# Performance work log

Measured on AMD Instinct MI355X. Metric: run time of the kernel, lower is better.

Reference implementation:

```python
import jax, jax.numpy as jnp
import numpy as np

S, B, I, H = 512, 128, 256, 512  # seq_len, batch, input_size, hidden_size


def setup_inputs() -> dict:
    key = jax.random.key(0)
    ks = jax.random.split(key, 5)
    # Gates stacked in order (f, i, o, c), each Linear init'd like nn.Linear
    lim_w = 1.0 / np.sqrt(I)
    lim_u = 1.0 / np.sqrt(H)
    x = jax.random.normal(ks[0], (S, B, I), dtype=jnp.float32)
    W = jax.random.uniform(ks[1], (4 * H, I), minval=-lim_w, maxval=lim_w, dtype=jnp.float32)
    bW = jax.random.uniform(ks[2], (4 * H,), minval=-lim_w, maxval=lim_w, dtype=jnp.float32)
    U = jax.random.uniform(ks[3], (4 * H, H), minval=-lim_u, maxval=lim_u, dtype=jnp.float32)
    bU = jax.random.uniform(ks[4], (4 * H,), minval=-lim_u, maxval=lim_u, dtype=jnp.float32)
    return {"x": x, "W": W, "bW": bW, "U": U, "bU": bU}


def reference(x, W, bW, U, bU):
    """LSTM over time-major x. Gates stacked (f, i, o, c) along dim 0 of W/U.
    Returns (h_seq [S,B,H], h_final [B,H], c_final [B,H]).
    The original's bf/bi/bo/bc buffers are zeros and thus omitted."""
    Hh = U.shape[1]
    # Input projection for all timesteps + both Linear biases, done once.
    xg = jnp.einsum('sbi,gi->sbg', x, W) + bW + bU  # [S, B, 4H]

    def step(carry, xg_t):
        h, c = carry
        g = xg_t + h @ U.T  # [B, 4H]
        f = jax.nn.sigmoid(g[:, 0 * Hh:1 * Hh])
        i = jax.nn.sigmoid(g[:, 1 * Hh:2 * Hh])
        o = jax.nn.sigmoid(g[:, 2 * Hh:3 * Hh])
        cand = jnp.tanh(g[:, 3 * Hh:4 * Hh])
        c_new = f * c + i * cand
        h_new = o * jnp.tanh(c_new)
        return (h_new, c_new), h_new

    b = x.shape[1]
    init = (jnp.zeros((b, Hh), x.dtype), jnp.zeros((b, Hh), x.dtype))
    (h_fin, c_fin), h_seq = jax.lax.scan(step, init, xg)
    return h_seq, h_fin, c_fin
```

## Files before the change

### kernel.cpp

```cpp
#include <hip/hip_runtime.h>
#include <hip/hip_bf16.h>


#define S_LEN 512
#define BATCH 128
#define ISZ   256
#define HSZ   512

typedef __attribute__((ext_vector_type(8))) short  s16x8;
typedef __attribute__((ext_vector_type(4))) float  f32x4;

#define FLAG_BYTES 4096
#define HOFF   4096
#define HBYTES ((size_t)2 * BATCH * HSZ * 2)
#define XOFF   (HOFF + HBYTES)
#define XBYTES ((size_t)S_LEN * BATCH * ISZ * 2)
#define WS_NEED (XOFF + XBYTES)

__device__ __forceinline__ unsigned short f2bf(float f) {
    unsigned u = __float_as_uint(f);
    u += 0x7fffu + ((u >> 16) & 1u);
    return (unsigned short)(u >> 16);
}

__device__ __forceinline__ s16x8 ld8f_bf(const float* p) {
    f32x4 a = *(const f32x4*)p;
    f32x4 b = *(const f32x4*)(p + 4);
    s16x8 r;
    r[0] = (short)f2bf(a[0]); r[1] = (short)f2bf(a[1]);
    r[2] = (short)f2bf(a[2]); r[3] = (short)f2bf(a[3]);
    r[4] = (short)f2bf(b[0]); r[5] = (short)f2bf(b[1]);
    r[6] = (short)f2bf(b[2]); r[7] = (short)f2bf(b[3]);
    return r;
}

__global__ void __launch_bounds__(256, 1)
cvt_x_kernel(const float* __restrict__ x, unsigned short* __restrict__ xbf, int n8) {
    int i = blockIdx.x * blockDim.x + threadIdx.x;
    const int stride = gridDim.x * blockDim.x;
    for (; i < n8; i += stride)
        *(s16x8*)(xbf + (size_t)i * 8) = ld8f_bf(x + (size_t)i * 8);
}

#define MFMA_BF16 __builtin_amdgcn_mfma_f32_16x16x32_bf16

template <bool BIGWS>
__global__ void __launch_bounds__(256, 1)
lstm_kq(const float* __restrict__ x,
        const float* __restrict__ W,
        const float* __restrict__ bW,
        const float* __restrict__ U,
        const float* __restrict__ bU,
        float* __restrict__ out,
        unsigned char* __restrict__ ws)
{
    __shared__ float g_lds[2][4][16][68];

    const int tid  = threadIdx.x;
    const int bid  = blockIdx.x;
    const int grp  = bid & 7;
    const int wg   = bid >> 3;
    const int jBase = wg * 16;
    const int rBase = grp * 16;

    unsigned* flags = (unsigned*)ws;
    unsigned short* h0 = (unsigned short*)(ws + HOFF);
    unsigned short* h1 = h0 + BATCH * HSZ;
    const unsigned short* xbf = (const unsigned short*)(ws + XOFF);

    const int kq   = tid >> 6;
    const int lane = tid & 63;
    const int l15  = lane & 15;
    const int lq   = lane >> 4;
    const int arow = rBase + l15;

    s16x8 ub[4][4], wb[4][2];
    float bias[4];
    #pragma unroll
    for (int n = 0; n < 4; ++n) {
        const int gRow = n * HSZ + jBase + l15;
        bias[n] = (kq == 0) ? (bW[gRow] + bU[gRow]) : 0.f;
        #pragma unroll
        for (int ki = 0; ki < 4; ++ki)
            ub[n][ki] = ld8f_bf(U + (size_t)gRow * HSZ + kq * 128 + ki * 32 + lq * 8);
        #pragma unroll
        for (int ki = 0; ki < 2; ++ki)
            wb[n][ki] = ld8f_bf(W + (size_t)gRow * ISZ + kq * 64 + ki * 32 + lq * 8);
    }

    const int er = tid >> 4, ej = tid & 15;
    const int orow = rBase + er, ocol = jBase + ej;
    float cst = 0.f;

    for (int t = 0; t < S_LEN; ++t) {
        const int par = t & 1;
        f32x4 acc[4] = { { bias[0], bias[0], bias[0], bias[0] },
                         { bias[1], bias[1], bias[1], bias[1] },
                         { bias[2], bias[2], bias[2], bias[2] },
                         { bias[3], bias[3], bias[3], bias[3] } };

        #pragma unroll
        for (int ki = 0; ki < 2; ++ki) {
            s16x8 a;
            if constexpr (BIGWS)
                a = *(const s16x8*)(xbf + ((size_t)t * BATCH + arow) * ISZ
                                    + kq * 64 + ki * 32 + lq * 8);
            else
                a = ld8f_bf(x + ((size_t)t * BATCH + arow) * ISZ
                            + kq * 64 + ki * 32 + lq * 8);
            #pragma unroll
            for (int n = 0; n < 4; ++n)
                acc[n] = MFMA_BF16(a, wb[n][ki], acc[n], 0, 0, 0);
        }

        if (t > 0) {
            const unsigned* fp = flags + grp * 128 + kq * 32 + (lane & 31);
            const unsigned tgt = (unsigned)t;
            for (;;) {
                unsigned v;
                asm volatile("global_load_dword %0, %1, off sc0 sc1\n\t"
                             "s_waitcnt vmcnt(0)" : "=v"(v) : "v"(fp) : "memory");
                if (__all(v >= tgt)) break;
            }
            __builtin_amdgcn_sched_barrier(0);

            const unsigned short* hp = (par ? h0 : h1)
                                       + (size_t)arow * HSZ + kq * 128 + lq * 8;
            s16x8 f0, f1, f2, f3;
#define LDH(d, o) asm volatile("global_load_dwordx4 %0, %1, off offset:" o " sc0 sc1" \
                               : "=v"(d) : "v"(hp) : "memory")
            LDH(f0, "0"); LDH(f1, "64"); LDH(f2, "128"); LDH(f3, "192");
#undef LDH
            asm volatile("s_waitcnt vmcnt(2)" ::: "memory");
            __builtin_amdgcn_sched_barrier(0);
            #pragma unroll
            for (int n = 0; n < 4; ++n)
                acc[n] = MFMA_BF16(f0, ub[n][0], acc[n], 0, 0, 0);
            #pragma unroll
            for (int n = 0; n < 4; ++n)
                acc[n] = MFMA_BF16(f1, ub[n][1], acc[n], 0, 0, 0);
            asm volatile("s_waitcnt vmcnt(0)" ::: "memory");
            __builtin_amdgcn_sched_barrier(0);
            #pragma unroll
            for (int n = 0; n < 4; ++n)
                acc[n] = MFMA_BF16(f2, ub[n][2], acc[n], 0, 0, 0);
            #pragma unroll
            for (int n = 0; n < 4; ++n)
                acc[n] = MFMA_BF16(f3, ub[n][3], acc[n], 0, 0, 0);
        }

        #pragma unroll
        for (int n = 0; n < 4; ++n)
            #pragma unroll
            for (int r = 0; r < 4; ++r)
                g_lds[par][kq][lq * 4 + r][n * 16 + l15] = acc[n][r];
        __syncthreads();

        const float gf = g_lds[par][0][er][ej]      + g_lds[par][1][er][ej]
                       + g_lds[par][2][er][ej]      + g_lds[par][3][er][ej];
        const float gi = g_lds[par][0][er][16 + ej] + g_lds[par][1][er][16 + ej]
                       + g_lds[par][2][er][16 + ej] + g_lds[par][3][er][16 + ej];
        const float go = g_lds[par][0][er][32 + ej] + g_lds[par][1][er][32 + ej]
                       + g_lds[par][2][er][32 + ej] + g_lds[par][3][er][32 + ej];
        const float gc = g_lds[par][0][er][48 + ej] + g_lds[par][1][er][48 + ej]
                       + g_lds[par][2][er][48 + ej] + g_lds[par][3][er][48 + ej];

        const float fg = 1.f / (1.f + __expf(-gf));
        const float ig = 1.f / (1.f + __expf(-gi));
        const float og = 1.f / (1.f + __expf(-go));
        const float ec = __expf(-2.f * fabsf(gc));
        const float cd = copysignf((1.f - ec) / (1.f + ec), gc);
        cst = fg * cst + ig * cd;
        const float eh = __expf(-2.f * fabsf(cst));
        const float hn = og * copysignf((1.f - eh) / (1.f + eh), cst);

        if (t < S_LEN - 1) {
            unsigned hv = (unsigned)f2bf(hn);
            unsigned short* hd = (par ? h1 : h0) + (size_t)orow * HSZ + ocol;
            asm volatile("global_store_short %0, %1, off sc0 sc1"
                         :: "v"(hd), "v"(hv) : "memory");
            asm volatile("s_waitcnt vmcnt(0)" ::: "memory");
            if (lane == 0) {
                unsigned* fl = flags + grp * 128 + wg * 4 + kq;
                unsigned ep = (unsigned)(t + 1);
                asm volatile("global_store_dword %0, %1, off sc0 sc1"
                             :: "v"(fl), "v"(ep) : "memory");
            }
            out[((size_t)t * BATCH + orow) * HSZ + ocol] = hn;
        } else {
            out[((size_t)t * BATCH + orow) * HSZ + ocol] = hn;
            const size_t HSEQ = (size_t)S_LEN * BATCH * HSZ;
            out[HSEQ + (size_t)orow * HSZ + ocol] = hn;
            out[HSEQ + (size_t)BATCH * HSZ + (size_t)orow * HSZ + ocol] = cst;
        }
    }
}

extern "C" void kernel_launch(void* const* d_in, const int* in_sizes, int n_in,
                              void* d_out, int out_size, void* d_ws, size_t ws_size,
                              hipStream_t stream) {
    const float* x  = (const float*)d_in[0];
    const float* W  = (const float*)d_in[1];
    const float* bW = (const float*)d_in[2];
    const float* U  = (const float*)d_in[3];
    const float* bU = (const float*)d_in[4];
    float* out = (float*)d_out;
    unsigned char* ws = (unsigned char*)d_ws;

    hipMemsetAsync(ws, 0, FLAG_BYTES, stream);

    void* args[] = { (void*)&x, (void*)&W, (void*)&bW, (void*)&U, (void*)&bU,
                     (void*)&out, (void*)&ws };

    if (ws_size >= WS_NEED) {
        const int n8 = S_LEN * BATCH * ISZ / 8;
        cvt_x_kernel<<<2048, 256, 0, stream>>>(x, (unsigned short*)(ws + XOFF), n8);
        hipError_t e = hipLaunchCooperativeKernel((void*)lstm_kq<true>, dim3(256),
                                                  dim3(256), args, 0, stream);
        if (e != hipSuccess)
            lstm_kq<true><<<dim3(256), dim3(256), 0, stream>>>(x, W, bW, U, bU, out, ws);
    } else {
        hipError_t e = hipLaunchCooperativeKernel((void*)lstm_kq<false>, dim3(256),
                                                  dim3(256), args, 0, stream);
        if (e != hipSuccess)
            lstm_kq<false><<<dim3(256), dim3(256), 0, stream>>>(x, W, bW, U, bU, out, ws);
    }
}
```

Baseline: 1.323 ms.

## Tag hidden-state words with timestep to validate data without store fences

Each hidden-state value is now stored as a 32-bit word: the bf16 value in the low half and the producing timestep in the high half. Consumers spin-load their h slice and check every tag against the expected step, then repack the low halves into bf16 MFMA operands. This removes the store wait that used to sit between the h store and the flag store. The cost is twice the h bytes on every step, an extra validation and repack pass, and clearing the larger workspace at launch. The old flag polling loop still runs before the tag check.

```diff
diff --git a/kernel.cpp b/kernel.cpp
--- a/kernel.cpp
+++ b/kernel.cpp
@@ -7,20 +7,32 @@
 #define ISZ   256
 #define HSZ   512
 
-typedef __attribute__((ext_vector_type(8))) short  s16x8;
-typedef __attribute__((ext_vector_type(4))) float  f32x4;
+typedef __attribute__((ext_vector_type(8))) short    s16x8;
+typedef __attribute__((ext_vector_type(4))) float    f32x4;
+typedef __attribute__((ext_vector_type(4))) unsigned u32x4;
+typedef __attribute__((ext_vector_type(4))) int      i32x4;
 
 #define FLAG_BYTES 4096
-#define HOFF   4096
-#define HBYTES ((size_t)2 * BATCH * HSZ * 2)
-#define XOFF   (HOFF + HBYTES)
-#define XBYTES ((size_t)S_LEN * BATCH * ISZ * 2)
+#define HOFF    4096
+#define HXWORDS ((size_t)BATCH * HSZ)
+#define HXBYTES ((size_t)2 * BATCH * HSZ * 4)
+#define XOFF    (HOFF + HXBYTES)
+#define XBYTES  ((size_t)S_LEN * BATCH * ISZ * 2)
 #define WS_NEED (XOFF + XBYTES)
 
 __device__ __forceinline__ unsigned short f2bf(float f) {
     unsigned u = __float_as_uint(f);
     u += 0x7fffu + ((u >> 16) & 1u);
     return (unsigned short)(u >> 16);
+}
+
+__device__ __forceinline__ unsigned permb(unsigned a, unsigned b, unsigned sel) {
+#if __has_builtin(__builtin_amdgcn_perm)
+    return __builtin_amdgcn_perm(a, b, sel);
+#else
+    if (sel == 0x01000504u) return (a & 0xFFFFu) | (b << 16);
+    else                    return (a >> 16) | (b & 0xFFFF0000u);
+#endif
 }
 
 __device__ __forceinline__ s16x8 ld8f_bf(const float* p) {
@@ -46,13 +58,13 @@
 
 template <bool BIGWS>
 __global__ void __launch_bounds__(256, 1)
-lstm_kq(const float* __restrict__ x,
-        const float* __restrict__ W,
-        const float* __restrict__ bW,
-        const float* __restrict__ U,
-        const float* __restrict__ bU,
-        float* __restrict__ out,
-        unsigned char* __restrict__ ws)
+lstm_tagflag(const float* __restrict__ x,
+             const float* __restrict__ W,
+             const float* __restrict__ bW,
+             const float* __restrict__ U,
+             const float* __restrict__ bU,
+             float* __restrict__ out,
+             unsigned char* __restrict__ ws)
 {
     __shared__ float g_lds[2][4][16][68];
 
@@ -64,8 +76,7 @@
     const int rBase = grp * 16;
 
     unsigned* flags = (unsigned*)ws;
-    unsigned short* h0 = (unsigned short*)(ws + HOFF);
-    unsigned short* h1 = h0 + BATCH * HSZ;
+    unsigned* hx    = (unsigned*)(ws + HOFF);
     const unsigned short* xbf = (const unsigned short*)(ws + XOFF);
 
     const int kq   = tid >> 6;
@@ -124,23 +135,42 @@
             }
             __builtin_amdgcn_sched_barrier(0);
 
-            const unsigned short* hp = (par ? h0 : h1)
-                                       + (size_t)arow * HSZ + kq * 128 + lq * 8;
-            s16x8 f0, f1, f2, f3;
-#define LDH(d, o) asm volatile("global_load_dwordx4 %0, %1, off offset:" o " sc0 sc1" \
+            const unsigned* hp = hx + (size_t)((t - 1) & 1) * HXWORDS
+                                 + (size_t)arow * HSZ + kq * 128 + lq * 8;
+            const unsigned tt = ((unsigned)t << 16) | (unsigned)t;
+            u32x4 L0, L1, L2, L3, L4, L5, L6, L7;
+            for (;;) {
+#define LDT(d, o) asm volatile("global_load_dwordx4 %0, %1, off offset:" o " sc0 sc1" \
                                : "=v"(d) : "v"(hp) : "memory")
-            LDH(f0, "0"); LDH(f1, "64"); LDH(f2, "128"); LDH(f3, "192");
-#undef LDH
-            asm volatile("s_waitcnt vmcnt(2)" ::: "memory");
-            __builtin_amdgcn_sched_barrier(0);
+                LDT(L0, "0");   LDT(L1, "16");
+                LDT(L2, "128"); LDT(L3, "144");
+                LDT(L4, "256"); LDT(L5, "272");
+                LDT(L6, "384"); LDT(L7, "400");
+#undef LDT
+                asm volatile("s_waitcnt vmcnt(0)" ::: "memory");
+                __builtin_amdgcn_sched_barrier(0);
+                unsigned bad = 0;
+#define TCHK(A) { bad |= permb(A[0], A[1], 0x03020706u) ^ tt; \
+                  bad |= permb(A[2], A[3], 0x03020706u) ^ tt; }
+                TCHK(L0) TCHK(L1) TCHK(L2) TCHK(L3)
+                TCHK(L4) TCHK(L5) TCHK(L6) TCHK(L7)
+#undef TCHK
+                if (__all(bad == 0)) break;
+                __builtin_amdgcn_s_sleep(1);
+            }
+
+#define PACK(A, B) __builtin_bit_cast(s16x8, (i32x4){ \
+        (int)permb(A[0], A[1], 0x01000504u), (int)permb(A[2], A[3], 0x01000504u), \
+        (int)permb(B[0], B[1], 0x01000504u), (int)permb(B[2], B[3], 0x01000504u) })
+            s16x8 f0 = PACK(L0, L1), f1 = PACK(L2, L3);
+            s16x8 f2 = PACK(L4, L5), f3 = PACK(L6, L7);
+#undef PACK
             #pragma unroll
             for (int n = 0; n < 4; ++n)
                 acc[n] = MFMA_BF16(f0, ub[n][0], acc[n], 0, 0, 0);
             #pragma unroll
             for (int n = 0; n < 4; ++n)
                 acc[n] = MFMA_BF16(f1, ub[n][1], acc[n], 0, 0, 0);
-            asm volatile("s_waitcnt vmcnt(0)" ::: "memory");
-            __builtin_amdgcn_sched_barrier(0);
             #pragma unroll
             for (int n = 0; n < 4; ++n)
                 acc[n] = MFMA_BF16(f2, ub[n][2], acc[n], 0, 0, 0);
@@ -175,11 +205,10 @@
         const float hn = og * copysignf((1.f - eh) / (1.f + eh), cst);
 
         if (t < S_LEN - 1) {
-            unsigned hv = (unsigned)f2bf(hn);
-            unsigned short* hd = (par ? h1 : h0) + (size_t)orow * HSZ + ocol;
-            asm volatile("global_store_short %0, %1, off sc0 sc1"
+            unsigned hv = ((unsigned)(t + 1) << 16) | (unsigned)f2bf(hn);
+            unsigned* hd = hx + (size_t)par * HXWORDS + (size_t)orow * HSZ + ocol;
+            asm volatile("global_store_dword %0, %1, off sc0 sc1"
                          :: "v"(hd), "v"(hv) : "memory");
-            asm volatile("s_waitcnt vmcnt(0)" ::: "memory");
             if (lane == 0) {
                 unsigned* fl = flags + grp * 128 + wg * 4 + kq;
                 unsigned ep = (unsigned)(t + 1);
@@ -207,7 +236,7 @@
     float* out = (float*)d_out;
     unsigned char* ws = (unsigned char*)d_ws;
 
-    hipMemsetAsync(ws, 0, FLAG_BYTES, stream);
+    hipMemsetAsync(ws, 0, HOFF + HXBYTES, stream);
 
     void* args[] = { (void*)&x, (void*)&W, (void*)&bW, (void*)&U, (void*)&bU,
                      (void*)&out, (void*)&ws };
@@ -215,14 +244,14 @@
     if (ws_size >= WS_NEED) {
         const int n8 = S_LEN * BATCH * ISZ / 8;
         cvt_x_kernel<<<2048, 256, 0, stream>>>(x, (unsigned short*)(ws + XOFF), n8);
-        hipError_t e = hipLaunchCooperativeKernel((void*)lstm_kq<true>, dim3(256),
+        hipError_t e = hipLaunchCooperativeKernel((void*)lstm_tagflag<true>, dim3(256),
                                                   dim3(256), args, 0, stream);
         if (e != hipSuccess)
-            lstm_kq<true><<<dim3(256), dim3(256), 0, stream>>>(x, W, bW, U, bU, out, ws);
+            lstm_tagflag<true><<<dim3(256), dim3(256), 0, stream>>>(x, W, bW, U, bU, out, ws);
     } else {
-        hipError_t e = hipLaunchCooperativeKernel((void*)lstm_kq<false>, dim3(256),
+        hipError_t e = hipLaunchCooperativeKernel((void*)lstm_tagflag<false>, dim3(256),
                                                   dim3(256), args, 0, stream);
         if (e != hipSuccess)
-            lstm_kq<false><<<dim3(256), dim3(256), 0, stream>>>(x, W, bW, U, bU, out, ws);
+            lstm_tagflag<false><<<dim3(256), dim3(256), 0, stream>>>(x, W, bW, U, bU, out, ws);
     }
 }
```

Result: slower. 1.504 ms (+13.7%).
